# Optimization experiments

Hardware: AMD Instinct MI355X
Metric: run time of the kernel (lower is better)

The kernel has to match this reference:

```python
import jax, jax.numpy as jnp
import numpy as np

EPS = 1e-12
CHAMFER_W, NORM_W, EDGE_W = 1.0, 0.1, 0.5


def setup_inputs() -> dict:
    key = jax.random.key(0)
    ks = jax.random.split(key, 6)
    B, V, F, N = 8, 6890, 13776, 4096
    return {
        "predicted_vertices": jax.random.normal(ks[0], (B, V, 3), jnp.float32),
        "predicted_faces": jax.random.randint(ks[1], (F, 3), 0, V),
        "gt_vertices": jax.random.normal(ks[2], (B, V, 3), jnp.float32),
        "gt_faces": jax.random.randint(ks[3], (F, 3), 0, V),
        "rand_pred": jax.random.uniform(ks[4], (B, N, 3), jnp.float32),
        "rand_gt": jax.random.uniform(ks[5], (B, N, 3), jnp.float32),
    }


def _sample_points(vertices, faces, rnd):
    """Area-weighted surface sampling. vertices [B,V,3], faces [F,3], rnd [B,N,3].
    Returns (points [B,N,3], normals [B,N,3])."""
    tri = vertices[:, faces]                       # [B,F,3,3]
    v0, v1, v2 = tri[:, :, 0], tri[:, :, 1], tri[:, :, 2]
    cross = jnp.cross(v1 - v0, v2 - v0)            # [B,F,3]
    cn = jnp.linalg.norm(cross, axis=-1)           # [B,F]
    area = 0.5 * cn
    normals = cross / (cn[..., None] + EPS)
    cdf = jnp.cumsum(area, axis=1)
    cdf = cdf / (cdf[:, -1:] + EPS)
    u, r1, r2 = rnd[..., 0], rnd[..., 1], rnd[..., 2]
    idx = jax.vmap(jnp.searchsorted)(cdf, u)       # [B,N] inverse-CDF face pick
    idx = jnp.clip(idx, 0, faces.shape[0] - 1)
    g = lambda x: jnp.take_along_axis(x, idx[..., None], axis=1)
    p0, p1, p2 = g(v0), g(v1), g(v2)
    su = jnp.sqrt(r1)[..., None]                   # sqrt trick -> uniform barycentric
    w0 = 1.0 - su
    w1 = su * (1.0 - r2[..., None])
    w2 = su * r2[..., None]
    return w0 * p0 + w1 * p1 + w2 * p2, g(normals)


def reference(predicted_vertices, predicted_faces, gt_vertices, gt_faces, rand_pred, rand_gt):
    # NOTE: faithful to the source, which samples BOTH clouds from the predicted
    # mesh (copy-paste bug): gt cloud = second independent sample of pred mesh.
    pc, pn = _sample_points(predicted_vertices, predicted_faces, rand_pred)
    gc, gn = _sample_points(predicted_vertices, predicted_faces, rand_gt)

    # squared-distance chamfer: [B,N,N]
    d = (jnp.sum(pc * pc, -1)[:, :, None]
         + jnp.sum(gc * gc, -1)[:, None, :]
         - 2.0 * jnp.einsum('bnd,bmd->bnm', pc, gc))
    dist1 = jnp.min(d, axis=2)
    dist2 = jnp.min(d, axis=1)
    chamfer_loss = jnp.mean(dist1) + jnp.mean(dist2)

    # normal loss: cosine mismatch with nearest-neighbor normals
    nn = jnp.argmin(d, axis=2)                     # [B,N]
    gn_nn = jnp.take_along_axis(gn, nn[..., None], axis=1)
    norm_loss = jnp.mean(1.0 - jnp.abs(jnp.sum(pn * gn_nn, axis=-1)))

    # edge loss: mean squared edge length over the 3 edges of every face
    pv, pf = predicted_vertices, predicted_faces
    e01 = pv[:, pf[:, 0]] - pv[:, pf[:, 1]]
    e12 = pv[:, pf[:, 1]] - pv[:, pf[:, 2]]
    e20 = pv[:, pf[:, 2]] - pv[:, pf[:, 0]]
    edge_loss = (jnp.mean(jnp.sum(e01 * e01, -1))
                 + jnp.mean(jnp.sum(e12 * e12, -1))
                 + jnp.mean(jnp.sum(e20 * e20, -1))) / 3.0

    return CHAMFER_W * chamfer_loss + NORM_W * norm_loss + EDGE_W * edge_loss
```

## Files before the change

kernel.cpp:

```cpp
#include <hip/hip_runtime.h>

#define EPSF 1e-12f
#define FLTMAX 3.402823466e+38f

constexpr int B = 8, V = 6890, F = 13776, N = 4096;
constexpr int BF = B * F;
constexpr int BN = B * N;
constexpr int CHUNK = 512;
constexpr int NCHUNK = (F + CHUNK - 1) / CHUNK;
constexpr int SCAN_BLOCKS = B * NCHUNK;

__device__ __forceinline__ unsigned enc_f(float f) {
  unsigned b = __float_as_uint(f);
  return (b & 0x80000000u) ? ~b : (b | 0x80000000u);
}
__device__ __forceinline__ float dec_f(unsigned u) {
  return (u & 0x80000000u) ? __uint_as_float(u & 0x7FFFFFFFu) : __uint_as_float(~u);
}

__device__ __forceinline__ float block_sum_256(float v, float* s4) {
  #pragma unroll
  for (int off = 32; off > 0; off >>= 1) v += __shfl_down(v, off, 64);
  __syncthreads();
  if ((threadIdx.x & 63) == 0) s4[threadIdx.x >> 6] = v;
  __syncthreads();
  return s4[0] + s4[1] + s4[2] + s4[3];
}

__device__ __forceinline__ float face_geom(const float* __restrict__ pv,
                                           const int* __restrict__ pf,
                                           int b, int f, float4* __restrict__ nrm4,
                                           float& es) {
  if (f >= F) return 0.f;
  int i0 = pf[f * 3 + 0], i1 = pf[f * 3 + 1], i2 = pf[f * 3 + 2];
  const float* vb = pv + (size_t)b * V * 3;
  float x0 = vb[i0 * 3 + 0], y0 = vb[i0 * 3 + 1], z0 = vb[i0 * 3 + 2];
  float x1 = vb[i1 * 3 + 0], y1 = vb[i1 * 3 + 1], z1 = vb[i1 * 3 + 2];
  float x2 = vb[i2 * 3 + 0], y2 = vb[i2 * 3 + 1], z2 = vb[i2 * 3 + 2];
  float ax = x1 - x0, ay = y1 - y0, az = z1 - z0;
  float bx = x2 - x0, by = y2 - y0, bz = z2 - z0;
  float cx = ay * bz - az * by;
  float cy = az * bx - ax * bz;
  float cz = ax * by - ay * bx;
  float cn = sqrtf(cx * cx + cy * cy + cz * cz);
  float inv = 1.f / (cn + EPSF);
  nrm4[(size_t)b * F + f] = make_float4(cx * inv, cy * inv, cz * inv, 0.f);
  float ex = x0 - x1, ey = y0 - y1, ez = z0 - z1;
  es += ex * ex + ey * ey + ez * ez;
  ex = x1 - x2; ey = y1 - y2; ez = z1 - z2;
  es += ex * ex + ey * ey + ez * ez;
  es += bx * bx + by * by + bz * bz;
  return 0.5f * cn;
}

__global__ __launch_bounds__(256) void scan_faces_kernel(
    const float* __restrict__ pv, const int* __restrict__ pf,
    float* __restrict__ cdf, float* __restrict__ csum, float4* __restrict__ nrm4,
    float* __restrict__ edgep,
    unsigned long long* __restrict__ best1, unsigned* __restrict__ best2,
    float* __restrict__ acc, unsigned* __restrict__ cnt) {
  __shared__ float wsum[4];
  __shared__ float s4[4];
  int b = blockIdx.x / NCHUNK, ck = blockIdx.x % NCHUNK;
  int lane = threadIdx.x & 63, wid = threadIdx.x >> 6;

  int gid = blockIdx.x * 256 + threadIdx.x;
  if (gid < BN) { best1[gid] = ~0ull; best2[gid] = ~0u; }
  if (gid < 2) acc[gid] = 0.f;
  if (gid == 2) *cnt = 0u;

  int f0 = ck * CHUNK + 2 * threadIdx.x;
  float es = 0.f;
  float a0 = face_geom(pv, pf, b, f0, nrm4, es);
  float a1 = face_geom(pv, pf, b, f0 + 1, nrm4, es);

  float ts = a0 + a1;
  float x = ts;
  #pragma unroll
  for (int off = 1; off < 64; off <<= 1) {
    float y = __shfl_up(x, off, 64);
    if (lane >= off) x += y;
  }
  if (lane == 63) wsum[wid] = x;
  __syncthreads();
  float woff = 0.f;
  for (int w = 0; w < wid; ++w) woff += wsum[w];
  float excl = woff + x - ts;
  size_t g0 = (size_t)b * F + f0;
  if (f0 < F) cdf[g0] = excl + a0;
  if (f0 + 1 < F) cdf[g0 + 1] = excl + ts;
  if (threadIdx.x == 255) csum[blockIdx.x] = woff + x;

  float te = block_sum_256(es, s4);
  if (threadIdx.x == 0) edgep[blockIdx.x] = te;
}

__global__ __launch_bounds__(256) void sample_kernel(
    const float* __restrict__ pv, const int* __restrict__ pf,
    const float* __restrict__ cdf, const float* __restrict__ csum,
    const float4* __restrict__ nrm4,
    const float* __restrict__ rp, const float* __restrict__ rg,
    float4* __restrict__ pc4, float4* __restrict__ pn4,
    float4* __restrict__ gc4, float4* __restrict__ gn4) {
  int idx = blockIdx.x * 256 + threadIdx.x;
  if (idx >= 2 * BN) return;
  int set = (idx >= BN) ? 1 : 0;
  int i = idx - set * BN;
  int b = i / N;
  const float* r = (set ? rg : rp) + (size_t)i * 3;
  float u = r[0], r1 = r[1], r2 = r[2];

  const float* cs = csum + b * NCHUNK;
  float total = 0.f;
  #pragma unroll
  for (int k2 = 0; k2 < NCHUNK; ++k2) total += cs[k2];
  float target = u * (total + EPSF);

  int k = 0;
  float s = cs[0];
  while (s < target && k < NCHUNK - 1) { ++k; s += cs[k]; }
  float prefix = s - cs[k];
  float t2 = target - prefix;

  const float* c = cdf + (size_t)b * F + k * CHUNK;
  int base = k * CHUNK;
  int lo = 0, hi = CHUNK;
  while (lo < hi) {
    int mid = (lo + hi) >> 1;
    float v = (base + mid < F) ? c[mid] : FLTMAX;
    if (v < t2) lo = mid + 1; else hi = mid;
  }
  int f = base + lo;
  if (f > F - 1) f = F - 1;

  int i0 = pf[f * 3 + 0], i1 = pf[f * 3 + 1], i2 = pf[f * 3 + 2];
  const float* vb = pv + (size_t)b * V * 3;
  float su = sqrtf(r1);
  float w0 = 1.f - su, w1 = su * (1.f - r2), w2 = su * r2;
  float px = w0 * vb[i0 * 3 + 0] + w1 * vb[i1 * 3 + 0] + w2 * vb[i2 * 3 + 0];
  float py = w0 * vb[i0 * 3 + 1] + w1 * vb[i1 * 3 + 1] + w2 * vb[i2 * 3 + 1];
  float pz = w0 * vb[i0 * 3 + 2] + w1 * vb[i1 * 3 + 2] + w2 * vb[i2 * 3 + 2];
  float4* pts = (set ? gc4 : pc4);
  float4* pns = (set ? gn4 : pn4);
  pts[i] = make_float4(px, py, pz, px * px + py * py + pz * pz);
  pns[i] = nrm4[(size_t)b * F + f];
}

__global__ __launch_bounds__(256, 8) void chamfer_kernel(
    const float4* __restrict__ pc4, const float4* __restrict__ gc4,
    unsigned long long* __restrict__ best1, unsigned* __restrict__ best2) {
  const bool is1 = blockIdx.x < 1024;
  const int blk = is1 ? blockIdx.x : blockIdx.x - 1024;
  const int b = blk >> 7;
  const int nchunk = (blk >> 3) & 15, mchunk = blk & 7;
  const int n = nchunk * 256 + threadIdx.x;
  const int mbase = mchunk * 512;
  const float4 p = (is1 ? pc4 : gc4)[(size_t)b * N + n];
  const float4* __restrict__ other = (is1 ? gc4 : pc4) + (size_t)b * N + mbase;
  const float qx = -2.f * p.x, qy = -2.f * p.y, qz = -2.f * p.z;
  const float pp = p.w;

  if (is1) {
    float bd0 = FLTMAX, bd1 = FLTMAX, bd2 = FLTMAX, bd3 = FLTMAX;
    int bi0 = 0, bi1 = 0, bi2 = 0, bi3 = 0;
    #pragma unroll 2
    for (int j = 0; j < 512; j += 4) {
      float4 t0 = other[j], t1 = other[j + 1], t2 = other[j + 2], t3 = other[j + 3];
      float d0 = fmaf(qx, t0.x, fmaf(qy, t0.y, fmaf(qz, t0.z, pp + t0.w)));
      float d1 = fmaf(qx, t1.x, fmaf(qy, t1.y, fmaf(qz, t1.z, pp + t1.w)));
      float d2 = fmaf(qx, t2.x, fmaf(qy, t2.y, fmaf(qz, t2.z, pp + t2.w)));
      float d3 = fmaf(qx, t3.x, fmaf(qy, t3.y, fmaf(qz, t3.z, pp + t3.w)));
      if (d0 < bd0) { bd0 = d0; bi0 = mbase + j; }
      if (d1 < bd1) { bd1 = d1; bi1 = mbase + j + 1; }
      if (d2 < bd2) { bd2 = d2; bi2 = mbase + j + 2; }
      if (d3 < bd3) { bd3 = d3; bi3 = mbase + j + 3; }
    }
    if (bd1 < bd0 || (bd1 == bd0 && bi1 < bi0)) { bd0 = bd1; bi0 = bi1; }
    if (bd3 < bd2 || (bd3 == bd2 && bi3 < bi2)) { bd2 = bd3; bi2 = bi3; }
    if (bd2 < bd0 || (bd2 == bd0 && bi2 < bi0)) { bd0 = bd2; bi0 = bi2; }
    unsigned long long key = ((unsigned long long)enc_f(bd0) << 32) | (unsigned)bi0;
    atomicMin(&best1[(size_t)b * N + n], key);
  } else {
    float bda = FLTMAX, bdb = FLTMAX;
    #pragma unroll 2
    for (int j = 0; j < 512; j += 4) {
      float4 t0 = other[j], t1 = other[j + 1], t2 = other[j + 2], t3 = other[j + 3];
      float d0 = fmaf(qx, t0.x, fmaf(qy, t0.y, fmaf(qz, t0.z, pp + t0.w)));
      float d1 = fmaf(qx, t1.x, fmaf(qy, t1.y, fmaf(qz, t1.z, pp + t1.w)));
      float d2 = fmaf(qx, t2.x, fmaf(qy, t2.y, fmaf(qz, t2.z, pp + t2.w)));
      float d3 = fmaf(qx, t3.x, fmaf(qy, t3.y, fmaf(qz, t3.z, pp + t3.w)));
      bda = fminf(fminf(d0, d1), bda);
      bdb = fminf(fminf(d2, d3), bdb);
    }
    atomicMin(&best2[(size_t)b * N + n], enc_f(fminf(bda, bdb)));
  }
}

__global__ __launch_bounds__(256) void finalize_kernel(
    const unsigned long long* __restrict__ best1, const unsigned* __restrict__ best2,
    const float4* __restrict__ pn4, const float4* __restrict__ gn4,
    const float* __restrict__ edgep,
    float* __restrict__ acc, unsigned* __restrict__ cnt, float* __restrict__ out) {
  __shared__ float s4[4];
  __shared__ unsigned ticket;
  int i = blockIdx.x * 256 + threadIdx.x;
  int b = i >> 12;
  unsigned long long k1 = best1[i];
  float d1 = dec_f((unsigned)(k1 >> 32));
  int m = (int)(unsigned)(k1 & 0xFFFFFFFFull);
  float d2 = dec_f(best2[i]);
  float4 a = pn4[i];
  float4 g = gn4[((size_t)b << 12) + m];
  float nl = 1.f - fabsf(a.x * g.x + a.y * g.y + a.z * g.z);
  float sd = block_sum_256(d1 + d2, s4);
  float sn = block_sum_256(nl, s4);
  if (threadIdx.x == 0) {
    atomicAdd(&acc[0], sd);
    atomicAdd(&acc[1], sn);
    __threadfence();
    ticket = atomicAdd(cnt, 1u);
  }
  __syncthreads();
  if (ticket == 127) {
    float e = (threadIdx.x < SCAN_BLOCKS) ? edgep[threadIdx.x] : 0.f;
    float te = block_sum_256(e, s4);
    if (threadIdx.x == 0) {
      float chamf = atomicAdd(&acc[0], 0.f);
      float nsum  = atomicAdd(&acc[1], 0.f);
      float inv_bn = 1.f / (float)BN;
      out[0] = chamf * inv_bn + 0.1f * (nsum * inv_bn) + 0.5f * (te / (3.f * (float)BF));
    }
  }
}

extern "C" void kernel_launch(void* const* d_in, const int* in_sizes, int n_in,
                              void* d_out, int out_size, void* d_ws, size_t ws_size,
                              hipStream_t stream) {
  const float* pv = (const float*)d_in[0];
  const int*   pf = (const int*)d_in[1];
  const float* rp = (const float*)d_in[4];
  const float* rg = (const float*)d_in[5];
  float* out = (float*)d_out;

  unsigned long long* best1 = (unsigned long long*)d_ws;
  unsigned* best2 = (unsigned*)(best1 + BN);
  float4* pc4  = (float4*)(best2 + BN);
  float4* pn4  = pc4 + BN;
  float4* gc4  = pn4 + BN;
  float4* gn4  = gc4 + BN;
  float4* nrm4 = gn4 + BN;
  float* cdf   = (float*)(nrm4 + BF);
  float* csum  = cdf + BF;
  float* edgep = csum + SCAN_BLOCKS;
  float* acc   = edgep + SCAN_BLOCKS;
  unsigned* cnt = (unsigned*)(acc + 2);

  scan_faces_kernel<<<SCAN_BLOCKS, 256, 0, stream>>>(pv, pf, cdf, csum, nrm4, edgep,
                                                     best1, best2, acc, cnt);
  sample_kernel<<<(2 * BN) / 256, 256, 0, stream>>>(pv, pf, cdf, csum, nrm4,
                                                    rp, rg, pc4, pn4, gc4, gn4);
  chamfer_kernel<<<2048, 256, 0, stream>>>(pc4, gc4, best1, best2);
  finalize_kernel<<<BN / 256, 256, 0, stream>>>(best1, best2, pn4, gn4, edgep,
                                                acc, cnt, out);
}
```

Before: 125.5 us.

## Fuse finalize into chamfer kernel and compute both directions per block

The chamfer kernel now handles both nearest-neighbour directions in one block, with each thread looping over 256 candidates per direction instead of 512 for one. The finalize step is folded in using per-row-group completion counters: the last of the 16 column blocks for a row group reads the atomically reduced minima and computes the chamfer and normal partial sums. A global ticket then picks the final block to add the edge term and write the output. This drops one kernel launch and interleaves two independent distance streams for more ILP, at the cost of extra atomics and fences and a larger per-thread working set.

```diff
diff --git a/kernel.cpp b/kernel.cpp
--- a/kernel.cpp
+++ b/kernel.cpp
@@ -9,6 +9,7 @@
 constexpr int CHUNK = 512;
 constexpr int NCHUNK = (F + CHUNK - 1) / CHUNK;
 constexpr int SCAN_BLOCKS = B * NCHUNK;
+constexpr int NGROUP = 128;
 
 __device__ __forceinline__ unsigned enc_f(float f) {
   unsigned b = __float_as_uint(f);
@@ -58,7 +59,7 @@
     float* __restrict__ cdf, float* __restrict__ csum, float4* __restrict__ nrm4,
     float* __restrict__ edgep,
     unsigned long long* __restrict__ best1, unsigned* __restrict__ best2,
-    float* __restrict__ acc, unsigned* __restrict__ cnt) {
+    float* __restrict__ acc, unsigned* __restrict__ cnt, unsigned* __restrict__ gcnt) {
   __shared__ float wsum[4];
   __shared__ float s4[4];
   int b = blockIdx.x / NCHUNK, ck = blockIdx.x % NCHUNK;
@@ -68,12 +69,12 @@
   if (gid < BN) { best1[gid] = ~0ull; best2[gid] = ~0u; }
   if (gid < 2) acc[gid] = 0.f;
   if (gid == 2) *cnt = 0u;
+  if (gid < NGROUP) gcnt[gid] = 0u;
 
   int f0 = ck * CHUNK + 2 * threadIdx.x;
   float es = 0.f;
   float a0 = face_geom(pv, pf, b, f0, nrm4, es);
   float a1 = face_geom(pv, pf, b, f0 + 1, nrm4, es);
-
   float ts = a0 + a1;
   float x = ts;
   #pragma unroll
@@ -148,87 +149,82 @@
 
 __global__ __launch_bounds__(256, 8) void chamfer_kernel(
     const float4* __restrict__ pc4, const float4* __restrict__ gc4,
-    unsigned long long* __restrict__ best1, unsigned* __restrict__ best2) {
-  const bool is1 = blockIdx.x < 1024;
-  const int blk = is1 ? blockIdx.x : blockIdx.x - 1024;
-  const int b = blk >> 7;
-  const int nchunk = (blk >> 3) & 15, mchunk = blk & 7;
-  const int n = nchunk * 256 + threadIdx.x;
-  const int mbase = mchunk * 512;
-  const float4 p = (is1 ? pc4 : gc4)[(size_t)b * N + n];
-  const float4* __restrict__ other = (is1 ? gc4 : pc4) + (size_t)b * N + mbase;
-  const float qx = -2.f * p.x, qy = -2.f * p.y, qz = -2.f * p.z;
-  const float pp = p.w;
-
-  if (is1) {
-    float bd0 = FLTMAX, bd1 = FLTMAX, bd2 = FLTMAX, bd3 = FLTMAX;
-    int bi0 = 0, bi1 = 0, bi2 = 0, bi3 = 0;
-    #pragma unroll 2
-    for (int j = 0; j < 512; j += 4) {
-      float4 t0 = other[j], t1 = other[j + 1], t2 = other[j + 2], t3 = other[j + 3];
-      float d0 = fmaf(qx, t0.x, fmaf(qy, t0.y, fmaf(qz, t0.z, pp + t0.w)));
-      float d1 = fmaf(qx, t1.x, fmaf(qy, t1.y, fmaf(qz, t1.z, pp + t1.w)));
-      float d2 = fmaf(qx, t2.x, fmaf(qy, t2.y, fmaf(qz, t2.z, pp + t2.w)));
-      float d3 = fmaf(qx, t3.x, fmaf(qy, t3.y, fmaf(qz, t3.z, pp + t3.w)));
-      if (d0 < bd0) { bd0 = d0; bi0 = mbase + j; }
-      if (d1 < bd1) { bd1 = d1; bi1 = mbase + j + 1; }
-      if (d2 < bd2) { bd2 = d2; bi2 = mbase + j + 2; }
-      if (d3 < bd3) { bd3 = d3; bi3 = mbase + j + 3; }
-    }
-    if (bd1 < bd0 || (bd1 == bd0 && bi1 < bi0)) { bd0 = bd1; bi0 = bi1; }
-    if (bd3 < bd2 || (bd3 == bd2 && bi3 < bi2)) { bd2 = bd3; bi2 = bi3; }
-    if (bd2 < bd0 || (bd2 == bd0 && bi2 < bi0)) { bd0 = bd2; bi0 = bi2; }
-    unsigned long long key = ((unsigned long long)enc_f(bd0) << 32) | (unsigned)bi0;
-    atomicMin(&best1[(size_t)b * N + n], key);
-  } else {
-    float bda = FLTMAX, bdb = FLTMAX;
-    #pragma unroll 2
-    for (int j = 0; j < 512; j += 4) {
-      float4 t0 = other[j], t1 = other[j + 1], t2 = other[j + 2], t3 = other[j + 3];
-      float d0 = fmaf(qx, t0.x, fmaf(qy, t0.y, fmaf(qz, t0.z, pp + t0.w)));
-      float d1 = fmaf(qx, t1.x, fmaf(qy, t1.y, fmaf(qz, t1.z, pp + t1.w)));
-      float d2 = fmaf(qx, t2.x, fmaf(qy, t2.y, fmaf(qz, t2.z, pp + t2.w)));
-      float d3 = fmaf(qx, t3.x, fmaf(qy, t3.y, fmaf(qz, t3.z, pp + t3.w)));
-      bda = fminf(fminf(d0, d1), bda);
-      bdb = fminf(fminf(d2, d3), bdb);
-    }
-    atomicMin(&best2[(size_t)b * N + n], enc_f(fminf(bda, bdb)));
-  }
-}
-
-__global__ __launch_bounds__(256) void finalize_kernel(
-    const unsigned long long* __restrict__ best1, const unsigned* __restrict__ best2,
     const float4* __restrict__ pn4, const float4* __restrict__ gn4,
     const float* __restrict__ edgep,
-    float* __restrict__ acc, unsigned* __restrict__ cnt, float* __restrict__ out) {
+    unsigned long long* __restrict__ best1, unsigned* __restrict__ best2,
+    float* __restrict__ acc, unsigned* __restrict__ cnt, unsigned* __restrict__ gcnt,
+    float* __restrict__ out) {
   __shared__ float s4[4];
-  __shared__ unsigned ticket;
-  int i = blockIdx.x * 256 + threadIdx.x;
-  int b = i >> 12;
-  unsigned long long k1 = best1[i];
-  float d1 = dec_f((unsigned)(k1 >> 32));
-  int m = (int)(unsigned)(k1 & 0xFFFFFFFFull);
-  float d2 = dec_f(best2[i]);
-  float4 a = pn4[i];
-  float4 g = gn4[((size_t)b << 12) + m];
-  float nl = 1.f - fabsf(a.x * g.x + a.y * g.y + a.z * g.z);
-  float sd = block_sum_256(d1 + d2, s4);
-  float sn = block_sum_256(nl, s4);
-  if (threadIdx.x == 0) {
-    atomicAdd(&acc[0], sd);
-    atomicAdd(&acc[1], sn);
+  __shared__ unsigned tk;
+  const int tid = threadIdx.x;
+  const int b = blockIdx.x >> 8;
+  const int nc = (blockIdx.x >> 4) & 15, mc = blockIdx.x & 15;
+  const int n = nc * 256 + tid;
+  const int mbase = mc * 256;
+  const size_t row = (size_t)b * N + n;
+
+  const float4 pa = pc4[row];
+  const float4 pb = gc4[row];
+  const float4* __restrict__ sa = gc4 + (size_t)b * N + mbase;
+  const float4* __restrict__ sb = pc4 + (size_t)b * N + mbase;
+  const float qax = -2.f * pa.x, qay = -2.f * pa.y, qaz = -2.f * pa.z;
+  const float qbx = -2.f * pb.x, qby = -2.f * pb.y, qbz = -2.f * pb.z;
+  const float ppa = pa.w, ppb = pb.w;
+
+  float ad0 = FLTMAX, ad1 = FLTMAX;
+  int ai0 = 0, ai1 = 0;
+  float bd0 = FLTMAX, bd1 = FLTMAX;
+  #pragma unroll 2
+  for (int j = 0; j < 256; j += 2) {
+    float4 ta0 = sa[j], ta1 = sa[j + 1];
+    float4 tb0 = sb[j], tb1 = sb[j + 1];
+    float da0 = fmaf(qax, ta0.x, fmaf(qay, ta0.y, fmaf(qaz, ta0.z, ppa + ta0.w)));
+    float da1 = fmaf(qax, ta1.x, fmaf(qay, ta1.y, fmaf(qaz, ta1.z, ppa + ta1.w)));
+    float db0 = fmaf(qbx, tb0.x, fmaf(qby, tb0.y, fmaf(qbz, tb0.z, ppb + tb0.w)));
+    float db1 = fmaf(qbx, tb1.x, fmaf(qby, tb1.y, fmaf(qbz, tb1.z, ppb + tb1.w)));
+    if (da0 < ad0) { ad0 = da0; ai0 = mbase + j; }
+    if (da1 < ad1) { ad1 = da1; ai1 = mbase + j + 1; }
+    bd0 = fminf(bd0, db0);
+    bd1 = fminf(bd1, db1);
+  }
+  if (ad1 < ad0 || (ad1 == ad0 && ai1 < ai0)) { ad0 = ad1; ai0 = ai1; }
+  unsigned long long key = ((unsigned long long)enc_f(ad0) << 32) | (unsigned)ai0;
+  atomicMin(&best1[row], key);
+  atomicMin(&best2[row], enc_f(fminf(bd0, bd1)));
+
+  __threadfence();
+  if (tid == 0) tk = atomicAdd(&gcnt[(b << 4) + nc], 1u);
+  __syncthreads();
+  if (tk == 15) {
     __threadfence();
-    ticket = atomicAdd(cnt, 1u);
-  }
-  __syncthreads();
-  if (ticket == 127) {
-    float e = (threadIdx.x < SCAN_BLOCKS) ? edgep[threadIdx.x] : 0.f;
-    float te = block_sum_256(e, s4);
-    if (threadIdx.x == 0) {
-      float chamf = atomicAdd(&acc[0], 0.f);
-      float nsum  = atomicAdd(&acc[1], 0.f);
-      float inv_bn = 1.f / (float)BN;
-      out[0] = chamf * inv_bn + 0.1f * (nsum * inv_bn) + 0.5f * (te / (3.f * (float)BF));
+    unsigned long long k1 = __hip_atomic_load(&best1[row], __ATOMIC_RELAXED,
+                                              __HIP_MEMORY_SCOPE_AGENT);
+    unsigned k2 = __hip_atomic_load(&best2[row], __ATOMIC_RELAXED,
+                                    __HIP_MEMORY_SCOPE_AGENT);
+    float d1 = dec_f((unsigned)(k1 >> 32));
+    int m = (int)(unsigned)(k1 & 0xFFFFFFFFull);
+    float d2 = dec_f(k2);
+    float4 a = pn4[row];
+    float4 g = gn4[((size_t)b << 12) + m];
+    float nl = 1.f - fabsf(a.x * g.x + a.y * g.y + a.z * g.z);
+    float sd = block_sum_256(d1 + d2, s4);
+    float sn = block_sum_256(nl, s4);
+    if (tid == 0) {
+      atomicAdd(&acc[0], sd);
+      atomicAdd(&acc[1], sn);
+      __threadfence();
+      tk = atomicAdd(cnt, 1u);
+    }
+    __syncthreads();
+    if (tk == NGROUP - 1) {
+      float e = (tid < SCAN_BLOCKS) ? edgep[tid] : 0.f;
+      float te = block_sum_256(e, s4);
+      if (tid == 0) {
+        float chamf = atomicAdd(&acc[0], 0.f);
+        float nsum  = atomicAdd(&acc[1], 0.f);
+        float inv_bn = 1.f / (float)BN;
+        out[0] = chamf * inv_bn + 0.1f * (nsum * inv_bn) + 0.5f * (te / (3.f * (float)BF));
+      }
     }
   }
 }
@@ -253,13 +249,13 @@
   float* csum  = cdf + BF;
   float* edgep = csum + SCAN_BLOCKS;
   float* acc   = edgep + SCAN_BLOCKS;
-  unsigned* cnt = (unsigned*)(acc + 2);
+  unsigned* cnt  = (unsigned*)(acc + 2);
+  unsigned* gcnt = cnt + 1;
 
   scan_faces_kernel<<<SCAN_BLOCKS, 256, 0, stream>>>(pv, pf, cdf, csum, nrm4, edgep,
-                                                     best1, best2, acc, cnt);
+                                                     best1, best2, acc, cnt, gcnt);
   sample_kernel<<<(2 * BN) / 256, 256, 0, stream>>>(pv, pf, cdf, csum, nrm4,
                                                     rp, rg, pc4, pn4, gc4, gn4);
-  chamfer_kernel<<<2048, 256, 0, stream>>>(pc4, gc4, best1, best2);
-  finalize_kernel<<<BN / 256, 256, 0, stream>>>(best1, best2, pn4, gn4, edgep,
-                                                acc, cnt, out);
-}
+  chamfer_kernel<<<2048, 256, 0, stream>>>(pc4, gc4, pn4, gn4, edgep,
+                                           best1, best2, acc, cnt, gcnt, out);
+}
```

After: 260.9 us. 2.08x slower.

## Compute chamfer distances once per tile and reduce both directions from it

Applied to the files above, without the earlier changes.

The chamfer kernel used to compute the distance matrix twice, once for row minima and once for column minima. It now uses 128x128 tiles with 8x8 register blocking, so each distance is computed once and feeds both the row and column minima, which are merged through shared memory before atomics. The row key packs a truncated float (low 12 bits dropped) with a 12-bit column index into one 32-bit word. This relies on non-negative distances and loses precision in d1, and any tiny negative distance from rounding would break the unsigned ordering. The threadfence is also replaced by an s_waitcnt in finalize.

```diff
diff --git a/kernel.cpp b/kernel.cpp
--- a/kernel.cpp
+++ b/kernel.cpp
@@ -9,14 +9,6 @@
 constexpr int CHUNK = 512;
 constexpr int NCHUNK = (F + CHUNK - 1) / CHUNK;
 constexpr int SCAN_BLOCKS = B * NCHUNK;
-
-__device__ __forceinline__ unsigned enc_f(float f) {
-  unsigned b = __float_as_uint(f);
-  return (b & 0x80000000u) ? ~b : (b | 0x80000000u);
-}
-__device__ __forceinline__ float dec_f(unsigned u) {
-  return (u & 0x80000000u) ? __uint_as_float(u & 0x7FFFFFFFu) : __uint_as_float(~u);
-}
 
 __device__ __forceinline__ float block_sum_256(float v, float* s4) {
   #pragma unroll
@@ -57,7 +49,7 @@
     const float* __restrict__ pv, const int* __restrict__ pf,
     float* __restrict__ cdf, float* __restrict__ csum, float4* __restrict__ nrm4,
     float* __restrict__ edgep,
-    unsigned long long* __restrict__ best1, unsigned* __restrict__ best2,
+    unsigned* __restrict__ best1, unsigned* __restrict__ best2,
     float* __restrict__ acc, unsigned* __restrict__ cnt) {
   __shared__ float wsum[4];
   __shared__ float s4[4];
@@ -65,7 +57,7 @@
   int lane = threadIdx.x & 63, wid = threadIdx.x >> 6;
 
   int gid = blockIdx.x * 256 + threadIdx.x;
-  if (gid < BN) { best1[gid] = ~0ull; best2[gid] = ~0u; }
+  if (gid < BN) { best1[gid] = 0xFFFFFFFFu; best2[gid] = 0xFFFFFFFFu; }
   if (gid < 2) acc[gid] = 0.f;
   if (gid == 2) *cnt = 0u;
 
@@ -73,7 +65,6 @@
   float es = 0.f;
   float a0 = face_geom(pv, pf, b, f0, nrm4, es);
   float a1 = face_geom(pv, pf, b, f0 + 1, nrm4, es);
-
   float ts = a0 + a1;
   float x = ts;
   #pragma unroll
@@ -146,69 +137,80 @@
   pns[i] = nrm4[(size_t)b * F + f];
 }
 
-__global__ __launch_bounds__(256, 8) void chamfer_kernel(
+__global__ __launch_bounds__(256, 4) void chamfer_kernel(
     const float4* __restrict__ pc4, const float4* __restrict__ gc4,
-    unsigned long long* __restrict__ best1, unsigned* __restrict__ best2) {
-  const bool is1 = blockIdx.x < 1024;
-  const int blk = is1 ? blockIdx.x : blockIdx.x - 1024;
-  const int b = blk >> 7;
-  const int nchunk = (blk >> 3) & 15, mchunk = blk & 7;
-  const int n = nchunk * 256 + threadIdx.x;
-  const int mbase = mchunk * 512;
-  const float4 p = (is1 ? pc4 : gc4)[(size_t)b * N + n];
-  const float4* __restrict__ other = (is1 ? gc4 : pc4) + (size_t)b * N + mbase;
-  const float qx = -2.f * p.x, qy = -2.f * p.y, qz = -2.f * p.z;
-  const float pp = p.w;
-
-  if (is1) {
-    float bd0 = FLTMAX, bd1 = FLTMAX, bd2 = FLTMAX, bd3 = FLTMAX;
-    int bi0 = 0, bi1 = 0, bi2 = 0, bi3 = 0;
-    #pragma unroll 2
-    for (int j = 0; j < 512; j += 4) {
-      float4 t0 = other[j], t1 = other[j + 1], t2 = other[j + 2], t3 = other[j + 3];
-      float d0 = fmaf(qx, t0.x, fmaf(qy, t0.y, fmaf(qz, t0.z, pp + t0.w)));
-      float d1 = fmaf(qx, t1.x, fmaf(qy, t1.y, fmaf(qz, t1.z, pp + t1.w)));
-      float d2 = fmaf(qx, t2.x, fmaf(qy, t2.y, fmaf(qz, t2.z, pp + t2.w)));
-      float d3 = fmaf(qx, t3.x, fmaf(qy, t3.y, fmaf(qz, t3.z, pp + t3.w)));
-      if (d0 < bd0) { bd0 = d0; bi0 = mbase + j; }
-      if (d1 < bd1) { bd1 = d1; bi1 = mbase + j + 1; }
-      if (d2 < bd2) { bd2 = d2; bi2 = mbase + j + 2; }
-      if (d3 < bd3) { bd3 = d3; bi3 = mbase + j + 3; }
+    unsigned* __restrict__ best1, unsigned* __restrict__ best2) {
+  const int tid = threadIdx.x;
+  const int b = blockIdx.x >> 10;
+  const int tn = (blockIdx.x >> 5) & 31;
+  const int tm = blockIdx.x & 31;
+  const int ty = tid >> 4, tx = tid & 15;
+  const int r0 = tn * 128 + ty * 8;
+  const int c0 = tm * 128 + tx * 8;
+  const float4* __restrict__ prow = pc4 + (size_t)b * N + r0;
+  const float4* __restrict__ gcol = gc4 + (size_t)b * N + c0;
+
+  float qx[8], qy[8], qz[8], pp[8];
+  float4 G[8];
+  #pragma unroll
+  for (int i = 0; i < 8; ++i) {
+    float4 p = prow[i];
+    qx[i] = -2.f * p.x; qy[i] = -2.f * p.y; qz[i] = -2.f * p.z; pp[i] = p.w;
+  }
+  #pragma unroll
+  for (int j = 0; j < 8; ++j) G[j] = gcol[j];
+
+  unsigned rkey[8], cbit[8];
+  #pragma unroll
+  for (int i = 0; i < 8; ++i) { rkey[i] = 0xFFFFFFFFu; cbit[i] = 0xFFFFFFFFu; }
+
+  #pragma unroll
+  for (int i = 0; i < 8; ++i) {
+    #pragma unroll
+    for (int j = 0; j < 8; ++j) {
+      float dp = fmaf(qx[i], G[j].x, fmaf(qy[i], G[j].y, fmaf(qz[i], G[j].z, G[j].w)));
+      float d  = dp + pp[i];
+      unsigned db = __float_as_uint(d);
+      rkey[i] = min(rkey[i], (db & 0xFFFFF000u) | (unsigned)(c0 + j));
+      cbit[j] = min(cbit[j], db);
     }
-    if (bd1 < bd0 || (bd1 == bd0 && bi1 < bi0)) { bd0 = bd1; bi0 = bi1; }
-    if (bd3 < bd2 || (bd3 == bd2 && bi3 < bi2)) { bd2 = bd3; bi2 = bi3; }
-    if (bd2 < bd0 || (bd2 == bd0 && bi2 < bi0)) { bd0 = bd2; bi0 = bi2; }
-    unsigned long long key = ((unsigned long long)enc_f(bd0) << 32) | (unsigned)bi0;
-    atomicMin(&best1[(size_t)b * N + n], key);
-  } else {
-    float bda = FLTMAX, bdb = FLTMAX;
-    #pragma unroll 2
-    for (int j = 0; j < 512; j += 4) {
-      float4 t0 = other[j], t1 = other[j + 1], t2 = other[j + 2], t3 = other[j + 3];
-      float d0 = fmaf(qx, t0.x, fmaf(qy, t0.y, fmaf(qz, t0.z, pp + t0.w)));
-      float d1 = fmaf(qx, t1.x, fmaf(qy, t1.y, fmaf(qz, t1.z, pp + t1.w)));
-      float d2 = fmaf(qx, t2.x, fmaf(qy, t2.y, fmaf(qz, t2.z, pp + t2.w)));
-      float d3 = fmaf(qx, t3.x, fmaf(qy, t3.y, fmaf(qz, t3.z, pp + t3.w)));
-      bda = fminf(fminf(d0, d1), bda);
-      bdb = fminf(fminf(d2, d3), bdb);
-    }
-    atomicMin(&best2[(size_t)b * N + n], enc_f(fminf(bda, bdb)));
+  }
+
+  __shared__ unsigned mrg[128][17];
+  #pragma unroll
+  for (int i = 0; i < 8; ++i) mrg[ty * 8 + i][tx] = rkey[i];
+  __syncthreads();
+  if (tid < 128) {
+    unsigned best = 0xFFFFFFFFu;
+    #pragma unroll
+    for (int k = 0; k < 16; ++k) best = min(best, mrg[tid][k]);
+    atomicMin(&best1[(size_t)b * N + tn * 128 + tid], best);
+  }
+  __syncthreads();
+  #pragma unroll
+  for (int j = 0; j < 8; ++j) mrg[tx * 8 + j][ty] = cbit[j];
+  __syncthreads();
+  if (tid < 128) {
+    unsigned best = 0xFFFFFFFFu;
+    #pragma unroll
+    for (int k = 0; k < 16; ++k) best = min(best, mrg[tid][k]);
+    atomicMin(&best2[(size_t)b * N + tm * 128 + tid], best);
   }
 }
 
 __global__ __launch_bounds__(256) void finalize_kernel(
-    const unsigned long long* __restrict__ best1, const unsigned* __restrict__ best2,
+    const unsigned* __restrict__ best1, const unsigned* __restrict__ best2,
     const float4* __restrict__ pn4, const float4* __restrict__ gn4,
     const float* __restrict__ edgep,
     float* __restrict__ acc, unsigned* __restrict__ cnt, float* __restrict__ out) {
   __shared__ float s4[4];
-  __shared__ unsigned ticket;
+  __shared__ unsigned tk;
   int i = blockIdx.x * 256 + threadIdx.x;
   int b = i >> 12;
-  unsigned long long k1 = best1[i];
-  float d1 = dec_f((unsigned)(k1 >> 32));
-  int m = (int)(unsigned)(k1 & 0xFFFFFFFFull);
-  float d2 = dec_f(best2[i]);
+  unsigned k1 = best1[i];
+  float d1 = __uint_as_float(k1 & 0xFFFFF000u);
+  int m = (int)(k1 & 0xFFFu);
+  float d2 = __uint_as_float(best2[i]);
   float4 a = pn4[i];
   float4 g = gn4[((size_t)b << 12) + m];
   float nl = 1.f - fabsf(a.x * g.x + a.y * g.y + a.z * g.z);
@@ -217,11 +219,11 @@
   if (threadIdx.x == 0) {
     atomicAdd(&acc[0], sd);
     atomicAdd(&acc[1], sn);
-    __threadfence();
-    ticket = atomicAdd(cnt, 1u);
-  }
-  __syncthreads();
-  if (ticket == 127) {
+    __asm__ __volatile__("s_waitcnt vmcnt(0)" ::: "memory");
+    tk = atomicAdd(cnt, 1u);
+  }
+  __syncthreads();
+  if (tk == 127) {
     float e = (threadIdx.x < SCAN_BLOCKS) ? edgep[threadIdx.x] : 0.f;
     float te = block_sum_256(e, s4);
     if (threadIdx.x == 0) {
@@ -242,8 +244,8 @@
   const float* rg = (const float*)d_in[5];
   float* out = (float*)d_out;
 
-  unsigned long long* best1 = (unsigned long long*)d_ws;
-  unsigned* best2 = (unsigned*)(best1 + BN);
+  unsigned* best1 = (unsigned*)d_ws;
+  unsigned* best2 = best1 + BN;
   float4* pc4  = (float4*)(best2 + BN);
   float4* pn4  = pc4 + BN;
   float4* gc4  = pn4 + BN;
@@ -259,7 +261,7 @@
                                                      best1, best2, acc, cnt);
   sample_kernel<<<(2 * BN) / 256, 256, 0, stream>>>(pv, pf, cdf, csum, nrm4,
                                                     rp, rg, pc4, pn4, gc4, gn4);
-  chamfer_kernel<<<2048, 256, 0, stream>>>(pc4, gc4, best1, best2);
+  chamfer_kernel<<<8 * 32 * 32, 256, 0, stream>>>(pc4, gc4, best1, best2);
   finalize_kernel<<<BN / 256, 256, 0, stream>>>(best1, best2, pn4, gn4, edgep,
                                                 acc, cnt, out);
 }
```

Measured after the change: 123.9 us. About the same (-1.3%).
